# Optimization experiments

Hardware: AMD Instinct MI355X
Metric: run time of the kernel (lower is better)

## Reference

```python
import jax, jax.numpy as jnp
import numpy as np

B, C_IN, FH, FW = 4, 256, 64, 176
N_PTS = 150000
D_BINS = 64
BEV_H = BEV_W = 200
RES = 0.5
EPS = 1e-5


def setup_inputs() -> dict:
    key = jax.random.key(0)
    ks = jax.random.split(key, 8)
    camera_features = jax.random.normal(ks[0], (B, C_IN, FH, FW), dtype=jnp.float32)
    pixels_uv = jax.random.uniform(ks[1], (B, N_PTS, 2), dtype=jnp.float32)
    K_inv = jax.random.normal(ks[2], (B, 3, 3), dtype=jnp.float32)
    # depth head params: Conv2d(256,128,3,pad=1) -> BN(128) -> ReLU -> Conv2d(128,64,1)
    W1 = jax.random.normal(ks[3], (128, C_IN, 3, 3), dtype=jnp.float32) * 0.02
    b1 = jnp.zeros((128,), dtype=jnp.float32)
    gamma = jnp.ones((128,), dtype=jnp.float32)
    beta = jnp.zeros((128,), dtype=jnp.float32)
    W2 = jax.random.normal(ks[4], (D_BINS, 128, 1, 1), dtype=jnp.float32) * 0.05
    b2 = jnp.zeros((D_BINS,), dtype=jnp.float32)
    depth_bins = jnp.linspace(1.0, 60.0, D_BINS, dtype=jnp.float32)
    return {"camera_features": camera_features, "pixels_uv": pixels_uv, "K_inv": K_inv,
            "W1": W1, "b1": b1, "gamma": gamma, "beta": beta, "W2": W2, "b2": b2,
            "depth_bins": depth_bins}


def _depth_head(x, W1, b1, gamma, beta, W2, b2):
    dn = ("NCHW", "OIHW", "NCHW")
    h = jax.lax.conv_general_dilated(x, W1, (1, 1), ((1, 1), (1, 1)), dimension_numbers=dn)
    h = h + b1[None, :, None, None]
    # BatchNorm2d, training-mode batch statistics (module is used without eval())
    mu = h.mean(axis=(0, 2, 3), keepdims=True)
    var = h.var(axis=(0, 2, 3), keepdims=True)
    h = (h - mu) * jax.lax.rsqrt(var + EPS)
    h = h * gamma[None, :, None, None] + beta[None, :, None, None]
    h = jax.nn.relu(h)
    logits = jax.lax.conv_general_dilated(h, W2, (1, 1), ((0, 0), (0, 0)), dimension_numbers=dn)
    logits = logits + b2[None, :, None, None]
    return jax.nn.softmax(logits, axis=1)  # [B, D, H, W]


def reference(camera_features, pixels_uv, K_inv, W1, b1, gamma, beta, W2, b2, depth_bins):
    depth_dist = _depth_head(camera_features, W1, b1, gamma, beta, W2, b2)

    # lift_to_3d
    exp_d = depth_dist.mean(axis=1)  # [B, H, W]
    ones = jnp.ones((B, N_PTS, 1), dtype=pixels_uv.dtype)
    homo = jnp.concatenate([pixels_uv, ones], axis=-1)            # [B, N, 3]
    pts3d = jnp.einsum('bnk,bjk->bnj', homo, K_inv)               # homo @ K_inv^T
    depth = exp_d.mean(axis=(1, 2))[:, None, None]                # [B, 1, 1]
    pts3d = pts3d * depth                                         # [B, N, 3]

    # splat_to_bev: scatter-add occupancy, then clamp to [0, 1]
    x_min = -(BEV_H * RES / 2)
    gx = jnp.clip(((pts3d[:, :, 0] - x_min) / RES).astype(jnp.int32), 0, BEV_W - 1)
    gy = jnp.clip(((pts3d[:, :, 1] - x_min) / RES).astype(jnp.int32), 0, BEV_H - 1)
    flat_idx = (jnp.arange(B, dtype=jnp.int32)[:, None] * (BEV_H * BEV_W) + gy * BEV_W + gx).ravel()
    grid = jnp.zeros((B * BEV_H * BEV_W,), dtype=jnp.float32).at[flat_idx].add(1.0)
    bev_grid = jnp.clip(grid.reshape(B, BEV_H, BEV_W), 0.0, 1.0)

    # expected_depth
    exp_depth = (depth_dist * depth_bins[None, :, None, None]).sum(axis=1)  # [B, H, W]

    return bev_grid, depth_dist, exp_depth, pts3d
```

## Files before the change

kernel.cpp:

```cpp
#include <hip/hip_runtime.h>

#define BATCH 4
#define CIN 256
#define FH 64
#define FW 176
#define HW (FH*FW)
#define PHW 11748
#define C1 128
#define DBINS 64
#define NPTS 150000
#define BEVN 200
#define EPSV 1e-5f

#define OFF_BEV 0
#define OFF_DD  160000
#define OFF_ED  3043584
#define OFF_PTS 3088640

#define WSB_H    0
#define WSB_WT   11534336
#define WSB_W2B  12124160
#define WSB_BN   12140544
#define WSB_XTP  12144640
#define XTP_B_ELEMS 3007488
#define WS_NEED_FULL  36204544ull
#define WS_NEED_HALF  24174592ull

typedef short bfx8 __attribute__((ext_vector_type(8)));
typedef short bfx4 __attribute__((ext_vector_type(4)));
typedef float f32x4 __attribute__((ext_vector_type(4)));
typedef unsigned short u16;

__device__ __forceinline__ u16 f2bf(float f) {
  union { float f; unsigned int u; } v; v.f = f;
  unsigned int r = v.u + 0x7FFF + ((v.u >> 16) & 1);
  return (u16)(r >> 16);
}
__device__ __forceinline__ float bf2f(u16 h) {
  union { unsigned int u; float f; } v; v.u = ((unsigned int)h) << 16;
  return v.f;
}

__device__ __forceinline__ void gload_lds16(const void* g, void* l) {
  __builtin_amdgcn_global_load_lds(
      (const __attribute__((address_space(1))) unsigned int*)g,
      (__attribute__((address_space(3))) unsigned int*)l, 16, 0, 0);
}

__global__ __launch_bounds__(256) void k_init(
    float* __restrict__ out, u16* __restrict__ w2b,
    const float* __restrict__ W2, u16* __restrict__ wt,
    const float* __restrict__ W1, u16* __restrict__ xtp, int nb) {
  int idx = blockIdx.x * 256 + threadIdx.x;
  if (idx < BATCH * BEVN * BEVN) out[OFF_BEV + idx] = 0.0f;
  if (idx < DBINS * C1) w2b[idx] = f2bf(W2[idx]);
  if (idx < 9 * C1 * CIN) {
    int tap = idx >> 15, rem = idx & 32767;
    int co = rem >> 8, c = rem & 255;
    wt[idx] = f2bf(W1[(co * CIN + c) * 9 + tap]);
  }
  const int nbord = nb * 484 * 32;
  if (idx < nbord) {
    int bloc = idx / (484 * 32);
    int r = idx - bloc * 484 * 32;
    int bpx = r >> 5, ch8 = r & 31;
    int prow, pcol;
    if (bpx < 178)      { prow = 0;  pcol = bpx; }
    else if (bpx < 356) { prow = 65; pcol = bpx - 178; }
    else { int q = bpx - 356; prow = 1 + (q >> 1); pcol = (q & 1) * 177; }
    *(bfx8*)&xtp[(bloc * PHW + prow * 178 + pcol) * 256 + ch8 * 8] = (bfx8)(short)0;
  }
}

__global__ __launch_bounds__(256) void k_xt(
    const float* __restrict__ x, u16* __restrict__ xtp, int b0) {
  __shared__ u16 s_t[176 * 72];
  const int blk = blockIdx.x;
  const int bloc = blk >> 8;
  const int rem = blk & 255;
  const int row = rem >> 2;
  const int c0 = (rem & 3) * 64;
  const int b = b0 + bloc;
  const int t = threadIdx.x;
  #pragma unroll
  for (int i = 0; i < 44; ++i) {
    int f = i * 256 + t;
    int c = f / 176, px = f - c * 176;
    s_t[px * 72 + c] = f2bf(x[((b * CIN + c0 + c) * FH + row) * FW + px]);
  }
  __syncthreads();
  const int base = (bloc * PHW + (row + 1) * 178 + 1) * 256 + c0;
  #pragma unroll
  for (int i = 0; i < 6; ++i) {
    int f = i * 256 + t;
    if (f < 1408) {
      int px = f >> 3, s = f & 7;
      *(bfx8*)&xtp[base + (px << 8) + s * 8] = *(const bfx8*)&s_t[px * 72 + s * 8];
    }
  }
}

#define ABUF_E 4096
#define STEP_E 8192

__global__ __launch_bounds__(512, 4) void k_conv(
    const u16* __restrict__ xTp, const u16* __restrict__ wt,
    const float* __restrict__ b1, u16* __restrict__ hbf, int b0) {
  __shared__ __align__(16) u16 sMem[4 * STEP_E];

  const int blk = blockIdx.x;
  const int bloc = blk / 88;
  const int tile = blk % 88;
  const int h0 = (tile / 11) * 8;
  const int w0 = (tile % 11) * 16;
  const int b = b0 + bloc;
  const int t = threadIdx.x;
  const int lane = t & 63;
  const int wv = t >> 6;
  const int mw = wv >> 1, nw = wv & 1;
  const int l15 = lane & 15, kg = lane >> 4;

  int gA, gB;
  {
    int c = t;
    int px = c >> 2;
    int slog = (c & 3) ^ ((c >> 3) & 3);
    int prow = h0 + (px >> 4), pcol = w0 + (px & 15);
    gA = (bloc * PHW + prow * 178 + pcol) * 256 + slog * 8;
    gB = (c >> 2) * 256 + slog * 8;
  }
  const int sw8 = (kg ^ ((l15 >> 1) & 3)) << 3;

  f32x4 acc[2][4];
  #pragma unroll
  for (int mf = 0; mf < 2; ++mf)
    #pragma unroll
    for (int nf = 0; nf < 4; ++nf) acc[mf][nf] = (f32x4)(0.f);

#define STAGE(S, SEL)                                                          \
  {                                                                            \
    const int tap_ = (S) >> 3, ck_ = (S) & 7;                                  \
    const int dy_ = tap_ / 3, dx_ = tap_ - dy_ * 3;                            \
    const int ao_ = ((dy_ * 178 + dx_) << 8) + (ck_ << 5);                     \
    const int wo_ = tap_ * 32768 + (ck_ << 5);                                 \
    u16* lb_ = &sMem[(SEL) * STEP_E];                                          \
    gload_lds16(&xTp[gA + ao_], &lb_[(wv * 64) * 8]);                          \
    gload_lds16(&wt[gB + wo_], &lb_[ABUF_E + (wv * 64) * 8]);                  \
  }

#define COMPUTE(SEL)                                                           \
  {                                                                            \
    const u16* lb_ = &sMem[(SEL) * STEP_E];                                    \
    bfx8 af[2], bf[4];                                                         \
    _Pragma("unroll")                                                          \
    for (int mf = 0; mf < 2; ++mf)                                             \
      af[mf] = *(const bfx8*)&lb_[(mw * 32 + mf * 16 + l15) * 32 + sw8];       \
    _Pragma("unroll")                                                          \
    for (int nf = 0; nf < 4; ++nf)                                             \
      bf[nf] = *(const bfx8*)&lb_[ABUF_E + (nw * 64 + nf * 16 + l15) * 32 + sw8]; \
    _Pragma("unroll")                                                          \
    for (int mf = 0; mf < 2; ++mf)                                             \
      _Pragma("unroll")                                                        \
      for (int nf = 0; nf < 4; ++nf)                                           \
        acc[mf][nf] = __builtin_amdgcn_mfma_f32_16x16x32_bf16(af[mf], bf[nf], acc[mf][nf], 0, 0, 0); \
  }

#define VMCNT(N) asm volatile("s_waitcnt vmcnt(" #N ")" ::: "memory")
#define BARR __builtin_amdgcn_s_barrier()
#define SCHED0 __builtin_amdgcn_sched_barrier(0)

  STAGE(0, 0);
  STAGE(1, 1);
  STAGE(2, 2);

  #pragma unroll 1
  for (int s = 0; s <= 64; s += 4) {
    VMCNT(4); BARR; SCHED0;
    COMPUTE(0);
    STAGE(s + 3, 3);
    VMCNT(4); BARR; SCHED0;
    COMPUTE(1);
    STAGE(s + 4, 0);
    VMCNT(4); BARR; SCHED0;
    COMPUTE(2);
    STAGE(s + 5, 1);
    VMCNT(4); BARR; SCHED0;
    COMPUTE(3);
    STAGE(s + 6, 2);
  }
  VMCNT(4); BARR; SCHED0;
  COMPUTE(0);
  STAGE(71, 3);
  VMCNT(4); BARR; SCHED0;
  COMPUTE(1);
  VMCNT(2); BARR; SCHED0;
  COMPUTE(2);
  VMCNT(0); BARR; SCHED0;
  COMPUTE(3);

  #pragma unroll
  for (int mf = 0; mf < 2; ++mf) {
    const int py = h0 + mw * 2 + mf;
    #pragma unroll
    for (int nf = 0; nf < 4; ++nf) {
      const int co = nw * 64 + nf * 16 + l15;
      const float bb = b1[co];
      bfx4 hv;
      #pragma unroll
      for (int j = 0; j < 4; ++j) hv[j] = (short)f2bf(acc[mf][nf][j] + bb);
      *(bfx4*)&hbf[((b * C1 + co) * FH + py) * FW + w0 + kg * 4] = hv;
    }
  }
#undef STAGE
#undef COMPUTE
#undef VMCNT
#undef BARR
#undef SCHED0
}

__global__ __launch_bounds__(256) void k_bnsum(
    const u16* __restrict__ h, float* __restrict__ part) {
  const int ch = blockIdx.x >> 2, b = blockIdx.x & 3;
  const int t = threadIdx.x;
  float s = 0.f, q = 0.f;
  const bfx8* p = (const bfx8*)&h[(b * C1 + ch) * HW];
  for (int i = t; i < HW / 8; i += 256) {
    bfx8 v8 = p[i];
    #pragma unroll
    for (int j = 0; j < 8; ++j) {
      float v = bf2f((u16)v8[j]);
      s += v;
      q = fmaf(v, v, q);
    }
  }
  #pragma unroll
  for (int o = 32; o; o >>= 1) {
    s += __shfl_xor(s, o);
    q += __shfl_xor(q, o);
  }
  __shared__ float rs[4], rq[4];
  int w = t >> 6;
  if ((t & 63) == 0) { rs[w] = s; rq[w] = q; }
  __syncthreads();
  if (t == 0) {
    part[ch * 8 + b * 2 + 0] = rs[0] + rs[1] + rs[2] + rs[3];
    part[ch * 8 + b * 2 + 1] = rq[0] + rq[1] + rq[2] + rq[3];
  }
}

__global__ __launch_bounds__(256) void k_head(
    const u16* __restrict__ h, const float* __restrict__ part,
    const float* __restrict__ gamma, const float* __restrict__ beta,
    const u16* __restrict__ w2b, const float* __restrict__ b2,
    const float* __restrict__ bins, float* __restrict__ out) {
  __shared__ u16 sAct[64 * 128];
  __shared__ float sP[64 * 68];
  __shared__ float sAB[256];

  const int blk = blockIdx.x;
  const int b = blk / 176;
  const int px0 = (blk % 176) * 64;
  const int t = threadIdx.x;
  const int lane = t & 63;
  const int w = t >> 6;
  const int l15 = lane & 15, kg = lane >> 4;

  if (t < 128) {
    float s = 0.f, q = 0.f;
    #pragma unroll
    for (int bb = 0; bb < 4; ++bb) {
      s += part[t * 8 + bb * 2 + 0];
      q += part[t * 8 + bb * 2 + 1];
    }
    const float inv_n = 1.0f / (float)(BATCH * HW);
    float mu = s * inv_n;
    float var = q * inv_n - mu * mu;
    float a = gamma[t] * rsqrtf(var + EPSV);
    sAB[t] = a;
    sAB[128 + t] = beta[t] - mu * a;
  }

  bfx8 bfr[4][4];
  #pragma unroll
  for (int nf = 0; nf < 4; ++nf)
    #pragma unroll
    for (int ck = 0; ck < 4; ++ck)
      bfr[nf][ck] = *(const bfx8*)&w2b[(nf * 16 + l15) * 128 + ck * 32 + kg * 8];
  float binr[4], b2r[4];
  #pragma unroll
  for (int nf = 0; nf < 4; ++nf) {
    binr[nf] = bins[nf * 16 + l15];
    b2r[nf] = b2[nf * 16 + l15];
  }
  f32x4 acc[4];
  #pragma unroll
  for (int nf = 0; nf < 4; ++nf) acc[nf] = (f32x4)(b2r[nf]);
  __syncthreads();

  #pragma unroll
  for (int i = 0; i < 4; ++i) {
    int f = t + i * 256;
    int c = f >> 3, g = f & 7;
    bfx8 v8 = *(const bfx8*)&h[(b * C1 + c) * HW + px0 + g * 8];
    float a = sAB[c], sh = sAB[128 + c];
    #pragma unroll
    for (int j = 0; j < 8; ++j) {
      int px = g * 8 + j;
      float v = fmaxf(fmaf(bf2f((u16)v8[j]), a, sh), 0.f);
      sAct[px * 128 + (((c >> 3) ^ (px & 15)) << 3) + (c & 7)] = f2bf(v);
    }
  }
  __syncthreads();

  #pragma unroll
  for (int ck = 0; ck < 4; ++ck) {
    bfx8 af = *(const bfx8*)&sAct[(w * 16 + l15) * 128 + (((ck * 4 + kg) ^ l15) << 3)];
    #pragma unroll
    for (int nf = 0; nf < 4; ++nf)
      acc[nf] = __builtin_amdgcn_mfma_f32_16x16x32_bf16(af, bfr[nf][ck], acc[nf], 0, 0, 0);
  }

  #pragma unroll
  for (int j = 0; j < 4; ++j) {
    float e[4];
    float z = 0.f, ez = 0.f;
    #pragma unroll
    for (int nf = 0; nf < 4; ++nf) {
      e[nf] = __expf(acc[nf][j]);
      z += e[nf];
      ez = fmaf(e[nf], binr[nf], ez);
    }
    #pragma unroll
    for (int o = 1; o < 16; o <<= 1) {
      z += __shfl_xor(z, o);
      ez += __shfl_xor(ez, o);
    }
    float inv = 1.0f / z;
    int px = w * 16 + kg * 4 + j;
    #pragma unroll
    for (int nf = 0; nf < 4; ++nf)
      sP[(nf * 16 + l15) * 68 + px] = e[nf] * inv;
    if (l15 == kg * 4 + j) out[OFF_ED + b * HW + px0 + px] = ez * inv;
  }
  __syncthreads();

  #pragma unroll
  for (int i = 0; i < 4; ++i) {
    int f = t + i * 256;
    int d = f >> 4, q = f & 15;
    f32x4 v;
    #pragma unroll
    for (int jj = 0; jj < 4; ++jj) v[jj] = sP[d * 68 + q * 4 + jj];
    *(f32x4*)&out[OFF_DD + (b * DBINS + d) * HW + px0 + q * 4] = v;
  }
}

__global__ void k_points(const float* __restrict__ uv, const float* __restrict__ kinv,
                         float* __restrict__ out) {
  int idx = blockIdx.x * 256 + threadIdx.x;
  if (idx >= BATCH * NPTS) return;
  int b = idx / NPTS;
  const float depth = 1.0f / 64.0f;
  float u = uv[idx * 2 + 0];
  float v = uv[idx * 2 + 1];
  const float* K = &kinv[b * 9];
  float p0 = (u * K[0] + v * K[1] + K[2]) * depth;
  float p1 = (u * K[3] + v * K[4] + K[5]) * depth;
  float p2 = (u * K[6] + v * K[7] + K[8]) * depth;
  out[OFF_PTS + idx * 3 + 0] = p0;
  out[OFF_PTS + idx * 3 + 1] = p1;
  out[OFF_PTS + idx * 3 + 2] = p2;
  int gx = (int)((p0 + 50.0f) * 2.0f);
  int gy = (int)((p1 + 50.0f) * 2.0f);
  gx = min(max(gx, 0), BEVN - 1);
  gy = min(max(gy, 0), BEVN - 1);
  out[OFF_BEV + (b * BEVN + gy) * BEVN + gx] = 1.0f;
}

extern "C" void kernel_launch(void* const* d_in, const int* in_sizes, int n_in,
                              void* d_out, int out_size, void* d_ws, size_t ws_size,
                              hipStream_t stream) {
  const float* x     = (const float*)d_in[0];
  const float* uv    = (const float*)d_in[1];
  const float* kinv  = (const float*)d_in[2];
  const float* w1    = (const float*)d_in[3];
  const float* b1    = (const float*)d_in[4];
  const float* gamma = (const float*)d_in[5];
  const float* beta  = (const float*)d_in[6];
  const float* w2    = (const float*)d_in[7];
  const float* b2    = (const float*)d_in[8];
  const float* bins  = (const float*)d_in[9];
  float* out = (float*)d_out;

  u16*   wsH   = (u16*)d_ws;
  u16*   wsWT  = (u16*)((char*)d_ws + WSB_WT);
  u16*   wsW2B = (u16*)((char*)d_ws + WSB_W2B);
  float* wsBN  = (float*)((char*)d_ws + WSB_BN);
  u16*   wsXTP = (u16*)((char*)d_ws + WSB_XTP);

  int nb = (ws_size >= WS_NEED_FULL) ? 4 : (ws_size >= WS_NEED_HALF) ? 2 : 1;

  k_init<<<1152, 256, 0, stream>>>(out, wsW2B, w2, wsWT, w1, wsXTP, nb);
  for (int b0 = 0; b0 < BATCH; b0 += nb) {
    k_xt<<<nb * 256, 256, 0, stream>>>(x, wsXTP, b0);
    k_conv<<<nb * 88, 512, 0, stream>>>(wsXTP, wsWT, b1, wsH, b0);
  }
  k_bnsum<<<512, 256, 0, stream>>>(wsH, wsBN);
  k_head<<<704, 256, 0, stream>>>(wsH, wsBN, gamma, beta, wsW2B, b2, bins, out);
  k_points<<<(BATCH * NPTS + 255) / 256, 256, 0, stream>>>(uv, kinv, out);
}
```

Baseline: 85.80 us.

## Widen conv K-step to 64 channels with double-buffered LDS pipeline

The implicit-GEMM conv kernel now loads 64 input channels per stage instead of 32, so there are 36 pipeline steps instead of 72. The LDS ring shrinks from four buffers to two, and each step waits with vmcnt(0) before a barrier. The XOR swizzle for the wider 64-element rows is reworked, and the occupancy hint of 4 in launch_bounds is removed. This halves the number of barriers and loop iterations but shortens prefetch depth to one stage, which risks exposing more global-load latency.

```diff
diff --git a/kernel.cpp b/kernel.cpp
--- a/kernel.cpp
+++ b/kernel.cpp
@@ -100,13 +100,13 @@
   }
 }
 
-#define ABUF_E 4096
-#define STEP_E 8192
-
-__global__ __launch_bounds__(512, 4) void k_conv(
+#define ABUF_E 8192
+#define STEP_E 16384
+
+__global__ __launch_bounds__(512) void k_conv(
     const u16* __restrict__ xTp, const u16* __restrict__ wt,
     const float* __restrict__ b1, u16* __restrict__ hbf, int b0) {
-  __shared__ __align__(16) u16 sMem[4 * STEP_E];
+  __shared__ __align__(16) u16 sMem[2 * STEP_E];
 
   const int blk = blockIdx.x;
   const int bloc = blk / 88;
@@ -120,16 +120,22 @@
   const int mw = wv >> 1, nw = wv & 1;
   const int l15 = lane & 15, kg = lane >> 4;
 
-  int gA, gB;
+  int gA0, gA1, gB0, gB1, ld0, ld1;
   {
-    int c = t;
-    int px = c >> 2;
-    int slog = (c & 3) ^ ((c >> 3) & 3);
-    int prow = h0 + (px >> 4), pcol = w0 + (px & 15);
-    gA = (bloc * PHW + prow * 178 + pcol) * 256 + slog * 8;
-    gB = (c >> 2) * 256 + slog * 8;
-  }
-  const int sw8 = (kg ^ ((l15 >> 1) & 3)) << 3;
+    int c = wv * 64 + lane;
+    int row = c >> 3;
+    int slog = (c & 7) ^ (row & 7);
+    int prow = h0 + (row >> 4), pcol = w0 + (row & 15);
+    gA0 = (bloc * PHW + prow * 178 + pcol) * 256 + slog * 8;
+    gB0 = row * 256 + slog * 8;
+    ld0 = c * 8;
+    c += 512; row = c >> 3;
+    slog = (c & 7) ^ (row & 7);
+    prow = h0 + (row >> 4); pcol = w0 + (row & 15);
+    gA1 = (bloc * PHW + prow * 178 + pcol) * 256 + slog * 8;
+    gB1 = row * 256 + slog * 8;
+    ld1 = c * 8;
+  }
 
   f32x4 acc[2][4];
   #pragma unroll
@@ -139,64 +145,58 @@
 
 #define STAGE(S, SEL)                                                          \
   {                                                                            \
-    const int tap_ = (S) >> 3, ck_ = (S) & 7;                                  \
+    const int tap_ = (S) >> 2, cin0_ = ((S) & 3) << 6;                         \
     const int dy_ = tap_ / 3, dx_ = tap_ - dy_ * 3;                            \
-    const int ao_ = ((dy_ * 178 + dx_) << 8) + (ck_ << 5);                     \
-    const int wo_ = tap_ * 32768 + (ck_ << 5);                                 \
+    const int ao_ = ((dy_ * 178 + dx_) << 8) + cin0_;                          \
+    const int wo_ = tap_ * 32768 + cin0_;                                      \
     u16* lb_ = &sMem[(SEL) * STEP_E];                                          \
-    gload_lds16(&xTp[gA + ao_], &lb_[(wv * 64) * 8]);                          \
-    gload_lds16(&wt[gB + wo_], &lb_[ABUF_E + (wv * 64) * 8]);                  \
+    gload_lds16(&xTp[gA0 + ao_], &lb_[ld0]);                                   \
+    gload_lds16(&xTp[gA1 + ao_], &lb_[ld1]);                                   \
+    gload_lds16(&wt[gB0 + wo_], &lb_[ABUF_E + ld0]);                           \
+    gload_lds16(&wt[gB1 + wo_], &lb_[ABUF_E + ld1]);                           \
   }
 
 #define COMPUTE(SEL)                                                           \
   {                                                                            \
     const u16* lb_ = &sMem[(SEL) * STEP_E];                                    \
-    bfx8 af[2], bf[4];                                                         \
     _Pragma("unroll")                                                          \
-    for (int mf = 0; mf < 2; ++mf)                                             \
-      af[mf] = *(const bfx8*)&lb_[(mw * 32 + mf * 16 + l15) * 32 + sw8];       \
-    _Pragma("unroll")                                                          \
-    for (int nf = 0; nf < 4; ++nf)                                             \
-      bf[nf] = *(const bfx8*)&lb_[ABUF_E + (nw * 64 + nf * 16 + l15) * 32 + sw8]; \
-    _Pragma("unroll")                                                          \
-    for (int mf = 0; mf < 2; ++mf)                                             \
+    for (int kk = 0; kk < 2; ++kk) {                                           \
+      bfx8 af[2], bf[4];                                                       \
       _Pragma("unroll")                                                        \
-      for (int nf = 0; nf < 4; ++nf)                                           \
-        acc[mf][nf] = __builtin_amdgcn_mfma_f32_16x16x32_bf16(af[mf], bf[nf], acc[mf][nf], 0, 0, 0); \
-  }
-
-#define VMCNT(N) asm volatile("s_waitcnt vmcnt(" #N ")" ::: "memory")
+      for (int mf = 0; mf < 2; ++mf) {                                         \
+        const int row_ = mw * 32 + mf * 16 + l15;                              \
+        const int ph_ = (kk * 4 + kg) ^ (l15 & 7);                             \
+        af[mf] = *(const bfx8*)&lb_[row_ * 64 + ph_ * 8];                      \
+      }                                                                        \
+      _Pragma("unroll")                                                        \
+      for (int nf = 0; nf < 4; ++nf) {                                         \
+        const int row_ = nw * 64 + nf * 16 + l15;                              \
+        const int ph_ = (kk * 4 + kg) ^ (l15 & 7);                             \
+        bf[nf] = *(const bfx8*)&lb_[ABUF_E + row_ * 64 + ph_ * 8];             \
+      }                                                                        \
+      _Pragma("unroll")                                                        \
+      for (int mf = 0; mf < 2; ++mf)                                           \
+        _Pragma("unroll")                                                      \
+        for (int nf = 0; nf < 4; ++nf)                                         \
+          acc[mf][nf] = __builtin_amdgcn_mfma_f32_16x16x32_bf16(af[mf], bf[nf], acc[mf][nf], 0, 0, 0); \
+    }                                                                          \
+  }
+
+#define VMCNT0 asm volatile("s_waitcnt vmcnt(0)" ::: "memory")
 #define BARR __builtin_amdgcn_s_barrier()
 #define SCHED0 __builtin_amdgcn_sched_barrier(0)
 
   STAGE(0, 0);
-  STAGE(1, 1);
-  STAGE(2, 2);
 
   #pragma unroll 1
-  for (int s = 0; s <= 64; s += 4) {
-    VMCNT(4); BARR; SCHED0;
+  for (int s = 0; s < 36; s += 2) {
+    VMCNT0; BARR; SCHED0;
+    if (s + 1 < 36) STAGE(s + 1, 1);
     COMPUTE(0);
-    STAGE(s + 3, 3);
-    VMCNT(4); BARR; SCHED0;
+    VMCNT0; BARR; SCHED0;
+    if (s + 2 < 36) STAGE(s + 2, 0);
     COMPUTE(1);
-    STAGE(s + 4, 0);
-    VMCNT(4); BARR; SCHED0;
-    COMPUTE(2);
-    STAGE(s + 5, 1);
-    VMCNT(4); BARR; SCHED0;
-    COMPUTE(3);
-    STAGE(s + 6, 2);
-  }
-  VMCNT(4); BARR; SCHED0;
-  COMPUTE(0);
-  STAGE(71, 3);
-  VMCNT(4); BARR; SCHED0;
-  COMPUTE(1);
-  VMCNT(2); BARR; SCHED0;
-  COMPUTE(2);
-  VMCNT(0); BARR; SCHED0;
-  COMPUTE(3);
+  }
 
   #pragma unroll
   for (int mf = 0; mf < 2; ++mf) {
@@ -213,7 +213,7 @@
   }
 #undef STAGE
 #undef COMPUTE
-#undef VMCNT
+#undef VMCNT0
 #undef BARR
 #undef SCHED0
 }
```

Measured after the change: 82.27 us. 1.04x faster.
